# Kernel optimization log

Hardware: AMD Instinct MI355X
Metric: run time of the kernel (lower is better)

Reference implementation:

```python
import jax, jax.numpy as jnp
import numpy as np

MARGIN = 0.2
MEM = 1000  # memory_size
EPS = 1e-12  # F.normalize eps


def _nearest_ds(x, h, w):
    # torch F.interpolate(mode='nearest'): src_idx = floor(dst_idx * H / h)
    B, H, W = x.shape
    ri = (jnp.arange(h) * H) // h
    ci = (jnp.arange(w) * W) // w
    return x[:, ri][:, :, ci]


def _first_k(mask, k):
    # Deterministic stand-in for randperm sampling: keep the first k True entries.
    rank = jnp.cumsum(mask.astype(jnp.int32)) - 1
    return mask & (rank < k), rank


def setup_inputs() -> dict:
    key = jax.random.key(0)
    k = jax.random.split(key, 6)
    B, C, H, W = 8, 21, 512, 512
    D, h, w = 128, 128, 128
    return {
        "preds": jax.random.normal(k[0], (B, C, H, W), jnp.float32),
        "embeddings": jax.random.normal(k[1], (B, D, h, w), jnp.float32),
        "gts": jax.random.randint(k[2], (B, H, W), 0, 21, dtype=jnp.int32),
        "fsss_gts": jax.random.randint(k[3], (B, H, W), 0, 256, dtype=jnp.int32),
        "pos_memory": jax.random.normal(k[4], (MEM, D), jnp.float32),
        "neg_memory": jax.random.normal(k[5], (MEM, D), jnp.float32),
    }


def reference(preds, embeddings, gts, fsss_gts, pos_memory, neg_memory):
    B, D, h, w = embeddings.shape
    M = pos_memory.shape[0]

    # downsample label maps / predicted classes to the feature resolution (nearest)
    s_pred = _nearest_ds(jnp.argmax(preds, axis=1).astype(jnp.float32), h, w).reshape(-1)
    s_fsss = _nearest_ds(fsss_gts.astype(jnp.float32), h, w).reshape(-1)
    # s_gt is computed in the original but unused for the loss.

    # L2-normalize embeddings over channel dim, flatten to [N, D] (channel-last)
    norm = jnp.sqrt(jnp.sum(embeddings * embeddings, axis=1, keepdims=True))
    emb = embeddings / jnp.maximum(norm, EPS)
    E = emb.transpose(1, 0, 2, 3).reshape(D, -1).T  # [N, D], N = B*h*w

    pred_mask = s_pred != 0
    fsss_mask = (s_fsss != 0) & (s_fsss != 255)
    ignore_mask = s_fsss == 255
    anchor_mask = pred_mask & fsss_mask
    positive_mask = fsss_mask ^ anchor_mask
    negative_mask = pred_mask ^ ((fsss_mask | ignore_mask) & pred_mask)

    sel_anc, _ = _first_k(anchor_mask, M // 10)
    sel_pos, rank_pos = _first_k(positive_mask, M // 3)
    sel_neg, rank_neg = _first_k(negative_mask, M // 3)

    # circular-buffer update (ptr=0): scatter selected (detached) embeddings into slots rank%M
    Ed = jax.lax.stop_gradient(E)
    idx_pos = jnp.where(sel_pos, rank_pos % M, M)  # M -> dropped
    idx_neg = jnp.where(sel_neg, rank_neg % M, M)
    pos_mem = pos_memory.at[idx_pos].set(Ed, mode='drop')
    neg_mem = neg_memory.at[idx_neg].set(Ed, mode='drop')

    # mean over all (anchor, memory) similarity pairs factorizes:
    # mean_{a,m} a.m = (sum_a a) . (sum_m m) / (Na * M)
    anc_sum = jnp.einsum('nd,n->d', E, sel_anc.astype(E.dtype))
    n_anc = jnp.maximum(jnp.sum(sel_anc.astype(E.dtype)), 1.0)
    pos_mean = jnp.dot(anc_sum, jnp.sum(pos_mem, axis=0)) / (n_anc * M)
    neg_mean = jnp.dot(anc_sum, jnp.sum(neg_mem, axis=0)) / (n_anc * M)

    return jax.nn.relu(pos_mean - neg_mean + MARGIN)
```

## Files before the change

### kernel.cpp

```cpp
#include <hip/hip_runtime.h>
#include <stdint.h>


#define NPOS  131072
#define NBLK  512
#define MEMSZ 1000
#define KANC  100
#define KPN   333
#define SLOT_POS 100
#define SLOT_NEG 433
#define FIX_SCALE 1099511627776.0
#define INV_FIX   (1.0 / 1099511627776.0)

#define OFF_FLAGS   0
#define OFF_COUNTS  131072
#define OFF_ACCUM   137216
#define OFF_CTR     149504

__global__ __launch_bounds__(256) void mask_kernel(
    const float* __restrict__ preds,
    const int* __restrict__ fsss,
    uint8_t* __restrict__ flags,
    int* __restrict__ blockCounts,
    unsigned long long* __restrict__ accum,
    unsigned int* __restrict__ counterB)
{
    const int tid = threadIdx.x, blk = blockIdx.x;
    const int lane = tid & 63, wave = tid >> 6;
    const int n = blk * 256 + tid;
    const int b = n >> 14;
    const int ij = n & 16383;
    const int row = (ij >> 7) << 2;
    const int col = (ij & 127) << 2;

    const float* p = preds + (size_t)b * 21 * 262144 + (size_t)row * 512 + col;
    float best = __builtin_nontemporal_load(p);
    int bc = 0;
#pragma unroll
    for (int c = 1; c < 21; ++c) {
        float v = __builtin_nontemporal_load(p + (size_t)c * 262144);
        if (v > best) { best = v; bc = c; }
    }
    const int fv = __builtin_nontemporal_load(
        fsss + (size_t)b * 262144 + (size_t)row * 512 + col);

    const bool pm = (bc != 0);
    const bool fm = (fv != 0) && (fv != 255);
    const int myflag = (int)(pm && fm)
                     | ((int)(!pm && fm) << 1)
                     | ((int)(pm && (fv == 0)) << 2);
    flags[n] = (uint8_t)myflag;

    __shared__ int s_i[12];
#pragma unroll
    for (int cat = 0; cat < 3; ++cat) {
        unsigned long long m = __ballot((myflag >> cat) & 1);
        if (lane == 0) s_i[cat * 4 + wave] = (int)__popcll(m);
    }
    __syncthreads();
    if (tid < 3)
        blockCounts[tid * NBLK + blk] =
            s_i[tid * 4] + s_i[tid * 4 + 1] + s_i[tid * 4 + 2] + s_i[tid * 4 + 3];

    if (blk == 0) {
        for (int i = tid; i < 4 * 3 * 128; i += 256) accum[i] = 0ull;
        if (tid == 0) *counterB = 0u;
    }
}

__global__ __launch_bounds__(256) void select_gather_final_kernel(
    const float* __restrict__ emb,
    const float* __restrict__ posMem,
    const float* __restrict__ negMem,
    const uint8_t* __restrict__ flags,
    const int* __restrict__ blockCounts,
    unsigned long long* __restrict__ accum,
    unsigned int* __restrict__ counterB,
    float* __restrict__ out)
{
    const int tid = threadIdx.x, blk = blockIdx.x;
    const int lane = tid & 63, wave = tid >> 6;

    __shared__ int s_pre[3 * NBLK];
    __shared__ int s_tot[3];
    __shared__ int s_w[4];
#pragma unroll 1
    for (int cat = 0; cat < 3; ++cat) {
        const int c0 = blockCounts[cat * NBLK + 2 * tid];
        const int c1 = blockCounts[cat * NBLK + 2 * tid + 1];
        const int pairsum = c0 + c1;
        int incl = pairsum;
#pragma unroll
        for (int off = 1; off < 64; off <<= 1) {
            int v = __shfl_up(incl, off, 64);
            if (lane >= off) incl += v;
        }
        if (lane == 63) s_w[wave] = incl;
        __syncthreads();
        int woff = 0;
#pragma unroll
        for (int w = 0; w < 4; ++w) if (w < wave) woff += s_w[w];
        const int excl0 = woff + incl - pairsum;
        s_pre[cat * NBLK + 2 * tid]     = excl0;
        s_pre[cat * NBLK + 2 * tid + 1] = excl0 + c0;
        if (tid == 0) s_tot[cat] = s_w[0] + s_w[1] + s_w[2] + s_w[3];
        __syncthreads();
    }
    const int A = min(KANC, s_tot[0]);
    const int P = min(KPN, s_tot[1]);
    const int Q = min(KPN, s_tot[2]);
    const int d = tid & 127;

    if (blk < 383) {
        __shared__ int s_nn[2];
        int nnv[2];
#pragma unroll 1
        for (int h = 0; h < 2; ++h) {
            const int slot = blk * 2 + h;
            int cat, r;
            if (slot < SLOT_POS)      { cat = 0; r = slot; }
            else if (slot < SLOT_NEG) { cat = 1; r = slot - SLOT_POS; }
            else                      { cat = 2; r = slot - SLOT_NEG; }
            const int cnt = (cat == 0) ? A : ((cat == 1) ? P : Q);
            if (r < cnt) {
                int lo = 0, hi = NBLK - 1;
                while (lo < hi) {
                    const int mid = (lo + hi + 1) >> 1;
                    if (s_pre[cat * NBLK + mid] <= r) lo = mid; else hi = mid - 1;
                }
                const int bb = lo;
                const int lr = r - s_pre[cat * NBLK + bb];
                const int bit = (flags[bb * 256 + tid] >> cat) & 1;
                const unsigned long long m = __ballot(bit);
                if (lane == 0) s_w[wave] = (int)__popcll(m);
                __syncthreads();
                int woff = 0;
#pragma unroll
                for (int w = 0; w < 4; ++w) if (w < wave) woff += s_w[w];
                const int intra = woff + (int)__popcll(m & ((1ull << lane) - 1ull));
                if (bit && intra == lr) s_nn[h] = bb * 256 + tid;
                __syncthreads();
                nnv[h] = s_nn[h];
            } else {
                nnv[h] = -1;
            }
        }

        const int half = tid >> 7;
        const int slot = blk * 2 + half;
        const int cat = (slot < SLOT_POS) ? 0 : ((slot < SLOT_NEG) ? 1 : 2);
        const int nn = nnv[half];
        float v = 0.f;
        if (nn >= 0)
            v = emb[((size_t)(nn >> 14) * 128 + d) * 16384 + (nn & 16383)];
        float sq = v * v;
#pragma unroll
        for (int off = 1; off < 64; off <<= 1) sq += __shfl_xor(sq, off, 64);
        __shared__ float s_f[4];
        if (lane == 0) s_f[wave] = sq;
        __syncthreads();
        const float nrm2 = s_f[half * 2] + s_f[half * 2 + 1];
        if (nn >= 0) {
            const float scale = 1.0f / fmaxf(sqrtf(nrm2), 1e-12f);
            const long long fx =
                (long long)llrint((double)v * (double)scale * FIX_SCALE);
            atomicAdd(&accum[(((blk & 3) * 3 + cat) << 7) + d],
                      (unsigned long long)fx);
        }
    } else {
        const int t = blk - 383;
        const int memSel = t >> 3;
        const int part = t & 7;
        const float* mem = memSel ? negMem : posMem;
        const int cnt = memSel ? Q : P;
        const int rowHalf = tid >> 7;
        const int m0 = part * 125;
        double acc = 0.0;
        for (int r = rowHalf; r < 125; r += 2) {
            const int m = m0 + r;
            if (m >= cnt) acc += (double)mem[(size_t)m * 128 + d];
        }
        const long long fx = (long long)llrint(acc * FIX_SCALE);
        atomicAdd(&accum[(((blk & 3) * 3 + (memSel ? 2 : 1)) << 7) + d],
                  (unsigned long long)fx);
    }

    __threadfence();
    __syncthreads();
    __shared__ int s_fin;
    if (tid == 0) {
        unsigned old = atomicAdd(counterB, 1u);
        s_fin = (old == 398) ? 1 : 0;
    }
    __syncthreads();
    if (!s_fin) return;
    __threadfence();

    __shared__ double s_d[2];
    if (tid < 128) {
        double anc = 0.0, pos = 0.0, neg = 0.0;
#pragma unroll
        for (int s = 0; s < 4; ++s) {
            anc += (double)(long long)accum[((s * 3 + 0) << 7) + tid];
            pos += (double)(long long)accum[((s * 3 + 1) << 7) + tid];
            neg += (double)(long long)accum[((s * 3 + 2) << 7) + tid];
        }
        double prod = anc * (pos - neg) * (INV_FIX * INV_FIX);
#pragma unroll
        for (int off = 1; off < 64; off <<= 1) prod += __shfl_xor(prod, off, 64);
        if (lane == 0) s_d[wave] = prod;
    }
    __syncthreads();
    if (tid == 0) {
        const double red = s_d[0] + s_d[1];
        const double nAnc = (A > 0) ? (double)A : 1.0;
        const double vv = red / (nAnc * (double)MEMSZ) + 0.2;
        out[0] = (float)(vv > 0.0 ? vv : 0.0);
    }
}

extern "C" void kernel_launch(void* const* d_in, const int* in_sizes, int n_in,
                              void* d_out, int out_size, void* d_ws, size_t ws_size,
                              hipStream_t stream) {
    const float* preds  = (const float*)d_in[0];
    const float* emb    = (const float*)d_in[1];
    const int* fsss     = (const int*)d_in[3];
    const float* posMem = (const float*)d_in[4];
    const float* negMem = (const float*)d_in[5];
    float* out = (float*)d_out;

    char* ws = (char*)d_ws;
    uint8_t* flags      = (uint8_t*)(ws + OFF_FLAGS);
    int* blockCounts    = (int*)(ws + OFF_COUNTS);
    unsigned long long* accum = (unsigned long long*)(ws + OFF_ACCUM);
    unsigned int* ctr   = (unsigned int*)(ws + OFF_CTR);

    mask_kernel<<<NBLK, 256, 0, stream>>>(preds, fsss, flags, blockCounts,
                                          accum, ctr);
    select_gather_final_kernel<<<399, 256, 0, stream>>>(emb, posMem, negMem,
                                                        flags, blockCounts,
                                                        accum, ctr, out);
}
```

Measured before the change: 49.11 us.

## Split argmax channels across four waves per pixel group, 2048 blocks

The mask kernel now assigns 64 pixels per block and spreads the 21 channel loads across four waves, each reducing five channels by max, then combines them through shared memory. This gives four times more blocks and more independent loads in flight for the latency-bound strided channel reads. Block counts grow to 2048 per category, so the scan in the second kernel handles eight entries per thread. The intra-block rank search becomes a single-wave ballot with no barrier. The argmax tie semantics change from first-max to a strict comparison against channel 0, which matches the reference's pred != 0 test.

```diff
diff --git a/kernel.cpp b/kernel.cpp
--- a/kernel.cpp
+++ b/kernel.cpp
@@ -2,11 +2,11 @@
 #include <stdint.h>
 
 
-#define NPOS  131072
-#define NBLK  512
-#define MEMSZ 1000
-#define KANC  100
-#define KPN   333
+#define NPOS   131072
+#define NBLK1  2048
+#define MEMSZ  1000
+#define KANC   100
+#define KPN    333
 #define SLOT_POS 100
 #define SLOT_NEG 433
 #define FIX_SCALE 1099511627776.0
@@ -14,8 +14,8 @@
 
 #define OFF_FLAGS   0
 #define OFF_COUNTS  131072
-#define OFF_ACCUM   137216
-#define OFF_CTR     149504
+#define OFF_ACCUM   155648
+#define OFF_CTR     167936
 
 __global__ __launch_bounds__(256) void mask_kernel(
     const float* __restrict__ preds,
@@ -27,40 +27,68 @@
 {
     const int tid = threadIdx.x, blk = blockIdx.x;
     const int lane = tid & 63, wave = tid >> 6;
-    const int n = blk * 256 + tid;
+    const int n = blk * 64 + lane;
     const int b = n >> 14;
     const int ij = n & 16383;
     const int row = (ij >> 7) << 2;
     const int col = (ij & 127) << 2;
 
-    const float* p = preds + (size_t)b * 21 * 262144 + (size_t)row * 512 + col;
-    float best = __builtin_nontemporal_load(p);
-    int bc = 0;
-#pragma unroll
-    for (int c = 1; c < 21; ++c) {
-        float v = __builtin_nontemporal_load(p + (size_t)c * 262144);
-        if (v > best) { best = v; bc = c; }
-    }
-    const int fv = __builtin_nontemporal_load(
-        fsss + (size_t)b * 262144 + (size_t)row * 512 + col);
-
-    const bool pm = (bc != 0);
-    const bool fm = (fv != 0) && (fv != 255);
-    const int myflag = (int)(pm && fm)
-                     | ((int)(!pm && fm) << 1)
-                     | ((int)(pm && (fv == 0)) << 2);
-    flags[n] = (uint8_t)myflag;
-
-    __shared__ int s_i[12];
-#pragma unroll
-    for (int cat = 0; cat < 3; ++cat) {
-        unsigned long long m = __ballot((myflag >> cat) & 1);
-        if (lane == 0) s_i[cat * 4 + wave] = (int)__popcll(m);
-    }
-    __syncthreads();
-    if (tid < 3)
-        blockCounts[tid * NBLK + blk] =
-            s_i[tid * 4] + s_i[tid * 4 + 1] + s_i[tid * 4 + 2] + s_i[tid * 4 + 3];
+    const float* base = preds + (size_t)b * 21 * 262144 + (size_t)row * 512 + col;
+#define LCH(c) __builtin_nontemporal_load(base + (size_t)(c) * 262144)
+
+    __shared__ float s_rest[4][64];
+    __shared__ float s_v00[64];
+    float mrest;
+    if (wave == 0) {
+        const float v00 = LCH(0);
+        s_v00[lane] = v00;
+        mrest = LCH(1);
+        mrest = fmaxf(mrest, LCH(2));
+        mrest = fmaxf(mrest, LCH(3));
+        mrest = fmaxf(mrest, LCH(4));
+        mrest = fmaxf(mrest, LCH(5));
+    } else if (wave == 1) {
+        mrest = LCH(6);
+        mrest = fmaxf(mrest, LCH(7));
+        mrest = fmaxf(mrest, LCH(8));
+        mrest = fmaxf(mrest, LCH(9));
+        mrest = fmaxf(mrest, LCH(10));
+    } else if (wave == 2) {
+        mrest = LCH(11);
+        mrest = fmaxf(mrest, LCH(12));
+        mrest = fmaxf(mrest, LCH(13));
+        mrest = fmaxf(mrest, LCH(14));
+        mrest = fmaxf(mrest, LCH(15));
+    } else {
+        mrest = LCH(16);
+        mrest = fmaxf(mrest, LCH(17));
+        mrest = fmaxf(mrest, LCH(18));
+        mrest = fmaxf(mrest, LCH(19));
+        mrest = fmaxf(mrest, LCH(20));
+    }
+#undef LCH
+    s_rest[wave][lane] = mrest;
+    __syncthreads();
+
+    if (wave == 0) {
+        const float mr = fmaxf(fmaxf(s_rest[0][lane], s_rest[1][lane]),
+                               fmaxf(s_rest[2][lane], s_rest[3][lane]));
+        const bool pm = mr > s_v00[lane];
+        const int fv = __builtin_nontemporal_load(
+            fsss + (size_t)b * 262144 + (size_t)row * 512 + col);
+        const bool fm = (fv != 0) && (fv != 255);
+        const int myflag = (int)(pm && fm)
+                         | ((int)(!pm && fm) << 1)
+                         | ((int)(pm && (fv == 0)) << 2);
+        flags[n] = (uint8_t)myflag;
+
+        const int ca = (int)__popcll(__ballot(myflag & 1));
+        const int cb = (int)__popcll(__ballot((myflag >> 1) & 1));
+        const int cc = (int)__popcll(__ballot((myflag >> 2) & 1));
+        if (lane == 0)      blockCounts[blk]            = ca;
+        else if (lane == 1) blockCounts[NBLK1 + blk]    = cb;
+        else if (lane == 2) blockCounts[2 * NBLK1 + blk] = cc;
+    }
 
     if (blk == 0) {
         for (int i = tid; i < 4 * 3 * 128; i += 256) accum[i] = 0ull;
@@ -80,16 +108,20 @@
 {
     const int tid = threadIdx.x, blk = blockIdx.x;
     const int lane = tid & 63, wave = tid >> 6;
-
-    __shared__ int s_pre[3 * NBLK];
+    const int d = tid & 127;
+
+    __shared__ int s_pre[3 * NBLK1];
     __shared__ int s_tot[3];
     __shared__ int s_w[4];
 #pragma unroll 1
     for (int cat = 0; cat < 3; ++cat) {
-        const int c0 = blockCounts[cat * NBLK + 2 * tid];
-        const int c1 = blockCounts[cat * NBLK + 2 * tid + 1];
-        const int pairsum = c0 + c1;
-        int incl = pairsum;
+        int e[8]; int sum = 0;
+#pragma unroll
+        for (int k = 0; k < 8; ++k) {
+            e[k] = blockCounts[cat * NBLK1 + tid * 8 + k];
+            sum += e[k];
+        }
+        int incl = sum;
 #pragma unroll
         for (int off = 1; off < 64; off <<= 1) {
             int v = __shfl_up(incl, off, 64);
@@ -100,22 +132,25 @@
         int woff = 0;
 #pragma unroll
         for (int w = 0; w < 4; ++w) if (w < wave) woff += s_w[w];
-        const int excl0 = woff + incl - pairsum;
-        s_pre[cat * NBLK + 2 * tid]     = excl0;
-        s_pre[cat * NBLK + 2 * tid + 1] = excl0 + c0;
+        int run = woff + incl - sum;
+#pragma unroll
+        for (int k = 0; k < 8; ++k) {
+            s_pre[cat * NBLK1 + tid * 8 + k] = run;
+            run += e[k];
+        }
         if (tid == 0) s_tot[cat] = s_w[0] + s_w[1] + s_w[2] + s_w[3];
         __syncthreads();
     }
     const int A = min(KANC, s_tot[0]);
     const int P = min(KPN, s_tot[1]);
     const int Q = min(KPN, s_tot[2]);
-    const int d = tid & 127;
 
     if (blk < 383) {
         __shared__ int s_nn[2];
-        int nnv[2];
-#pragma unroll 1
-        for (int h = 0; h < 2; ++h) {
+        if (tid < 2) s_nn[tid] = -1;
+        __syncthreads();
+        if (wave < 2) {
+            const int h = wave;
             const int slot = blk * 2 + h;
             int cat, r;
             if (slot < SLOT_POS)      { cat = 0; r = slot; }
@@ -123,33 +158,25 @@
             else                      { cat = 2; r = slot - SLOT_NEG; }
             const int cnt = (cat == 0) ? A : ((cat == 1) ? P : Q);
             if (r < cnt) {
-                int lo = 0, hi = NBLK - 1;
+                int lo = 0, hi = NBLK1 - 1;
                 while (lo < hi) {
                     const int mid = (lo + hi + 1) >> 1;
-                    if (s_pre[cat * NBLK + mid] <= r) lo = mid; else hi = mid - 1;
+                    if (s_pre[cat * NBLK1 + mid] <= r) lo = mid; else hi = mid - 1;
                 }
                 const int bb = lo;
-                const int lr = r - s_pre[cat * NBLK + bb];
-                const int bit = (flags[bb * 256 + tid] >> cat) & 1;
+                const int lr = r - s_pre[cat * NBLK1 + bb];
+                const int bit = (flags[bb * 64 + lane] >> cat) & 1;
                 const unsigned long long m = __ballot(bit);
-                if (lane == 0) s_w[wave] = (int)__popcll(m);
-                __syncthreads();
-                int woff = 0;
-#pragma unroll
-                for (int w = 0; w < 4; ++w) if (w < wave) woff += s_w[w];
-                const int intra = woff + (int)__popcll(m & ((1ull << lane) - 1ull));
-                if (bit && intra == lr) s_nn[h] = bb * 256 + tid;
-                __syncthreads();
-                nnv[h] = s_nn[h];
-            } else {
-                nnv[h] = -1;
+                const int intra = (int)__popcll(m & ((1ull << lane) - 1ull));
+                if (bit && intra == lr) s_nn[h] = bb * 64 + lane;
             }
         }
+        __syncthreads();
 
         const int half = tid >> 7;
         const int slot = blk * 2 + half;
         const int cat = (slot < SLOT_POS) ? 0 : ((slot < SLOT_NEG) ? 1 : 2);
-        const int nn = nnv[half];
+        const int nn = s_nn[half];
         float v = 0.f;
         if (nn >= 0)
             v = emb[((size_t)(nn >> 14) * 128 + d) * 16384 + (nn & 16383)];
@@ -235,8 +262,8 @@
     unsigned long long* accum = (unsigned long long*)(ws + OFF_ACCUM);
     unsigned int* ctr   = (unsigned int*)(ws + OFF_CTR);
 
-    mask_kernel<<<NBLK, 256, 0, stream>>>(preds, fsss, flags, blockCounts,
-                                          accum, ctr);
+    mask_kernel<<<NBLK1, 256, 0, stream>>>(preds, fsss, flags, blockCounts,
+                                           accum, ctr);
     select_gather_final_kernel<<<399, 256, 0, stream>>>(emb, posMem, negMem,
                                                         flags, blockCounts,
                                                         accum, ctr, out);
```

Result: slower. 50.33 us (+2.5%).
